# Kernel tuning notes

Measured on AMD Instinct MI355X. Metric: run time of the kernel, lower is better.

Reference implementation:

```python
import jax, jax.numpy as jnp
import numpy as np

ALPHA = 2
BETA = 4
# np.finfo(float64).eps threshold used in gaussian2D (max is always 1.0 at center)
EPS64 = 2.220446049250313e-16
CLIP = 1e-4


def _splat_level(boxes, labels, B, C, H, W):
    # boxes: [B,N,4] normalized cxcywh; labels: [B,N] int class ids
    # centers/radius in feature coordinates (scale_x*orig_w cancels to W)
    x = jnp.floor(boxes[..., 0] * W).astype(jnp.int32)           # [B,N]
    y = jnp.floor(boxes[..., 1] * H).astype(jnp.int32)
    bw = boxes[..., 2] * W
    bh = boxes[..., 3] * H
    r = jnp.maximum(1, jnp.floor((bw + bh) / 4.0).astype(jnp.int32))  # int() truncation, positive -> floor
    sigma = (2 * r + 1).astype(jnp.float32) / 6.0                # sigma = diameter/6

    dx = jnp.arange(W, dtype=jnp.int32)[None, None, :] - x[..., None]   # [B,N,W]
    dy = jnp.arange(H, dtype=jnp.int32)[None, None, :] - y[..., None]   # [B,N,H]
    d2 = (dx * dx)[:, :, None, :] + (dy * dy)[:, :, :, None]            # [B,N,H,W]
    g = jnp.exp(-d2.astype(jnp.float32) / (2.0 * sigma * sigma)[..., None, None])
    # window |d|<=r (border clipping is implicit since pixels lie in [0,W)x[0,H))
    inwin = (jnp.abs(dx) <= r[..., None])[:, :, None, :] & (jnp.abs(dy) <= r[..., None])[:, :, :, None]
    g = jnp.where(inwin & (g >= EPS64), g, 0.0)

    # scatter-max per (batch, label) channel
    N = boxes.shape[1]
    sid = (labels.astype(jnp.int32) + C * jnp.arange(B, dtype=jnp.int32)[:, None]).reshape(-1)  # [B*N]
    tm = jax.ops.segment_max(g.reshape(B * N, H * W), sid, num_segments=B * C)
    return jnp.maximum(tm, 0.0).reshape(B, C, H * W)  # empty segments (-inf) -> 0 init


def _forward(h0, h1, h2, boxes, labels):
    B, C = h0.shape[0], h0.shape[1]
    bx = jax.lax.stop_gradient(boxes)  # target construction is non-differentiable in the original
    maps = [h0, h1, h2]
    target = jnp.concatenate([_splat_level(bx, labels, B, C, m.shape[-2], m.shape[-1]) for m in maps], axis=2)
    heat = jnp.concatenate([m.reshape(B, C, -1) for m in maps], axis=2)

    pos = (target == 1.0).astype(heat.dtype)
    neg = (target < 1.0).astype(heat.dtype)
    neg_w = jnp.power(1.0 - target, BETA)
    p = jnp.clip(jax.nn.sigmoid(heat), CLIP, 1.0 - CLIP)
    pos_loss = jnp.log(p) * jnp.power(1.0 - p, ALPHA) * pos
    neg_loss = jnp.log(1.0 - p) * jnp.power(p, ALPHA) * neg_w * neg

    num_pos = pos.sum(axis=2, keepdims=True)
    pl = pos_loss.sum(axis=2, keepdims=True)
    nl = neg_loss.sum(axis=2, keepdims=True)
    safe = jnp.where(num_pos == 0, 1.0, num_pos)
    loss = jnp.where(num_pos == 0, -nl, -(pl + nl) / safe)
    loss = jnp.minimum(loss, 10.0)
    lm = jnp.log1p(loss.mean())
    return lm / (1.0 + lm)


def setup_inputs() -> dict:
    key = jax.random.key(0)
    k0, k1, k2, kb, kl = jax.random.split(key, 5)
    B, N, C = 8, 32, 80
    heat_map0 = jax.random.normal(k0, (B, C, 128, 128), dtype=jnp.float32)
    heat_map1 = jax.random.normal(k1, (B, C, 64, 64), dtype=jnp.float32)
    heat_map2 = jax.random.normal(k2, (B, C, 32, 32), dtype=jnp.float32)
    u = jax.random.uniform(kb, (B, N, 4), dtype=jnp.float32)
    boxes = jnp.concatenate([0.05 + 0.9 * u[..., :2], 0.02 + 0.4 * u[..., 2:]], axis=-1)
    labels = jax.random.randint(kl, (B, N), 0, C, dtype=jnp.int32)
    image_sizes = jnp.full((B, 2), 1024, dtype=jnp.int64)
    return {"heat_map0": heat_map0, "heat_map1": heat_map1, "heat_map2": heat_map2,
            "boxes": boxes, "labels": labels, "image_sizes": image_sizes}


def reference(heat_map0, heat_map1, heat_map2, boxes, labels, image_sizes):
    # image_sizes cancels out in the original math (scale_x * orig_w == feature W)
    return _forward(heat_map0, heat_map1, heat_map2, boxes, labels)
```

## Files before the change

### kernel.cpp

```cpp
#include <hip/hip_runtime.h>


#define BATCH 8
#define NBOX 32
#define NCH 80
#define NPLANE 640
#define NBLK 3840

__device__ __forceinline__ float sigmoid_clip(float h) {
    const float e = __expf(-h);
    float p = __builtin_amdgcn_rcpf(1.0f + e);
    return fminf(fmaxf(p, 1e-4f), 1.0f - 1e-4f);
}

__global__ __launch_bounds__(256) void splat_focal_kernel(
    const float* __restrict__ h0, const float* __restrict__ h1,
    const float* __restrict__ h2,
    const float* __restrict__ boxes, const int* __restrict__ labels,
    float* __restrict__ part)
{
    const int bid = blockIdx.x;
    const int tid = threadIdx.x;

    int plane, log2W, px_count, base_global, inpl_base;
    const float* heat;
    if (bid < 4 * NPLANE) {
        plane = bid >> 2;
        const int chunk = bid & 3;
        log2W = 7; heat = h0; px_count = 4096;
        inpl_base = chunk * 4096;
        base_global = plane * 16384 + inpl_base;
    } else if (bid < 5 * NPLANE) {
        plane = bid - 4 * NPLANE;
        log2W = 6; heat = h1; px_count = 4096;
        inpl_base = 0;
        base_global = plane * 4096;
    } else {
        plane = bid - 5 * NPLANE;
        log2W = 5; heat = h2; px_count = 1024;
        inpl_base = 0;
        base_global = plane * 1024;
    }
    const int W = 1 << log2W;
    const int b = plane / NCH;
    const int c = plane - b * NCH;

    __shared__ int s_k;
    __shared__ int s_x[NBOX], s_y[NBOX], s_r[NBOX];
    __shared__ float s_i2[NBOX];
    if (tid == 0) s_k = 0;
    __syncthreads();
    if (tid < NBOX) {
        if (labels[b * NBOX + tid] == c) {
            const float* bx = boxes + (b * NBOX + tid) * 4;
            const float fW = (float)W;
            int xi = (int)floorf(bx[0] * fW);
            int yi = (int)floorf(bx[1] * fW);
            int r = max(1, (int)floorf((bx[2] + bx[3]) * fW * 0.25f));
            float sigma = (float)(2 * r + 1) * (1.0f / 6.0f);
            int j = atomicAdd(&s_k, 1);
            s_x[j] = xi; s_y[j] = yi; s_r[j] = r;
            s_i2[j] = 1.0f / (2.0f * sigma * sigma);
        }
    }
    __syncthreads();
    const int k = s_k;

    float np_ = 0.0f, pl_ = 0.0f, nl_ = 0.0f;
    const int nf4 = px_count >> 2;
    const float4* hp = (const float4*)(heat + base_global);

    if (k == 0) {
        for (int i = tid; i < nf4; i += 256) {
            const float4 hq = hp[i];
            const float hv[4] = {hq.x, hq.y, hq.z, hq.w};
            #pragma unroll
            for (int j2 = 0; j2 < 4; ++j2) {
                const float p = sigmoid_clip(hv[j2]);
                nl_ += __logf(1.0f - p) * p * p;
            }
        }
    } else {
        for (int i = tid; i < nf4; i += 256) {
            const float4 hq = hp[i];
            const int off = inpl_base + (i << 2);
            const int py = off >> log2W;
            const int px0 = off & (W - 1);

            float t0 = 0.0f, t1 = 0.0f, t2 = 0.0f, t3 = 0.0f;
            for (int j = 0; j < k; ++j) {
                const int xj = s_x[j], yj = s_y[j], rj = s_r[j];
                const float i2 = s_i2[j];
                const int dy = py - yj;
                if (dy < -rj || dy > rj) continue;
                const float fdy2 = (float)(dy * dy);
                int dx = px0 - xj;
                if (dx >= -rj && dx <= rj)
                    t0 = fmaxf(t0, __expf(-((float)(dx * dx) + fdy2) * i2));
                dx += 1;
                if (dx >= -rj && dx <= rj)
                    t1 = fmaxf(t1, __expf(-((float)(dx * dx) + fdy2) * i2));
                dx += 1;
                if (dx >= -rj && dx <= rj)
                    t2 = fmaxf(t2, __expf(-((float)(dx * dx) + fdy2) * i2));
                dx += 1;
                if (dx >= -rj && dx <= rj)
                    t3 = fmaxf(t3, __expf(-((float)(dx * dx) + fdy2) * i2));
            }

            const float hv[4] = {hq.x, hq.y, hq.z, hq.w};
            const float tv[4] = {t0, t1, t2, t3};
            #pragma unroll
            for (int j2 = 0; j2 < 4; ++j2) {
                const float p = sigmoid_clip(hv[j2]);
                const float t = tv[j2];
                if (t == 1.0f) {
                    const float omp = 1.0f - p;
                    pl_ += __logf(p) * omp * omp;
                    np_ += 1.0f;
                } else {
                    const float omt = 1.0f - t;
                    const float nw = (omt * omt) * (omt * omt);
                    nl_ += __logf(1.0f - p) * p * p * nw;
                }
            }
        }
    }

    for (int o = 32; o > 0; o >>= 1) {
        np_ += __shfl_down(np_, o, 64);
        pl_ += __shfl_down(pl_, o, 64);
        nl_ += __shfl_down(nl_, o, 64);
    }
    __shared__ float s_np[4], s_pl[4], s_nl[4];
    const int wave = tid >> 6, lane = tid & 63;
    if (lane == 0) { s_np[wave] = np_; s_pl[wave] = pl_; s_nl[wave] = nl_; }
    __syncthreads();
    if (tid == 0) {
        part[bid]            = s_np[0] + s_np[1] + s_np[2] + s_np[3];
        part[NBLK + bid]     = s_pl[0] + s_pl[1] + s_pl[2] + s_pl[3];
        part[2 * NBLK + bid] = s_nl[0] + s_nl[1] + s_nl[2] + s_nl[3];
    }
}

__global__ __launch_bounds__(256) void finalize_kernel(
    const float* __restrict__ part, float* __restrict__ out)
{
    const int tid = threadIdx.x;
    const float* np = part;
    const float* pl = part + NBLK;
    const float* nl = part + 2 * NBLK;

    float s = 0.0f;
    for (int p = tid; p < NPLANE; p += 256) {
        const float4 n4 = ((const float4*)np)[p];
        const float4 p4 = ((const float4*)pl)[p];
        const float4 l4 = ((const float4*)nl)[p];
        const float a  = n4.x + n4.y + n4.z + n4.w + np[2560 + p] + np[3200 + p];
        const float ps = p4.x + p4.y + p4.z + p4.w + pl[2560 + p] + pl[3200 + p];
        const float ns = l4.x + l4.y + l4.z + l4.w + nl[2560 + p] + nl[3200 + p];
        const float loss = (a == 0.0f) ? (-ns) : (-(ps + ns) / a);
        s += fminf(loss, 10.0f);
    }
    for (int o = 32; o > 0; o >>= 1) s += __shfl_down(s, o, 64);
    __shared__ float sw[4];
    const int wave = tid >> 6, lane = tid & 63;
    if (lane == 0) sw[wave] = s;
    __syncthreads();
    if (tid == 0) {
        const float mean = (sw[0] + sw[1] + sw[2] + sw[3]) * (1.0f / (float)NPLANE);
        const float lm = log1pf(mean);
        out[0] = lm / (1.0f + lm);
    }
}

extern "C" void kernel_launch(void* const* d_in, const int* in_sizes, int n_in,
                              void* d_out, int out_size, void* d_ws, size_t ws_size,
                              hipStream_t stream) {
    const float* h0 = (const float*)d_in[0];
    const float* h1 = (const float*)d_in[1];
    const float* h2 = (const float*)d_in[2];
    const float* boxes = (const float*)d_in[3];
    const int* labels = (const int*)d_in[4];

    float* part = (float*)d_ws;

    splat_focal_kernel<<<NBLK, 256, 0, stream>>>(h0, h1, h2, boxes, labels, part);
    finalize_kernel<<<1, 256, 0, stream>>>(part, (float*)d_out);
}
```

Baseline: 101.5 us.

## Split dense negative-loss pass from sparse per-box window corrections

Every plane now runs a uniform streaming pass that computes only the unweighted negative term for all pixels. Separate per-box blocks visit just each box's window and add delta corrections for positive and weighted-negative pixels, using ownership by lowest box index to avoid double counting. The finalize kernel gathers the per-box corrections by label. This removes the per-pixel box loop and branch divergence from the dense pass, at the cost of more blocks, scattered window reads and recomputing box parameters inside the inner loop.

```diff
diff --git a/kernel.cpp b/kernel.cpp
--- a/kernel.cpp
+++ b/kernel.cpp
@@ -5,124 +5,117 @@
 #define NBOX 32
 #define NCH 80
 #define NPLANE 640
-#define NBLK 3840
 
-__device__ __forceinline__ float sigmoid_clip(float h) {
+__device__ __forceinline__ float sigclip(float h) {
     const float e = __expf(-h);
-    float p = __builtin_amdgcn_rcpf(1.0f + e);
+    const float p = __builtin_amdgcn_rcpf(1.0f + e);
     return fminf(fmaxf(p, 1e-4f), 1.0f - 1e-4f);
 }
+__device__ __forceinline__ float negterm(float h) {
+    const float p = sigclip(h);
+    return __logf(1.0f - p) * p * p;
+}
 
-__global__ __launch_bounds__(256) void splat_focal_kernel(
+__global__ __launch_bounds__(256) void hough_main_kernel(
     const float* __restrict__ h0, const float* __restrict__ h1,
     const float* __restrict__ h2,
     const float* __restrict__ boxes, const int* __restrict__ labels,
-    float* __restrict__ part)
+    float* __restrict__ ws)
 {
     const int bid = blockIdx.x;
     const int tid = threadIdx.x;
 
-    int plane, log2W, px_count, base_global, inpl_base;
-    const float* heat;
-    if (bid < 4 * NPLANE) {
-        plane = bid >> 2;
-        const int chunk = bid & 3;
-        log2W = 7; heat = h0; px_count = 4096;
-        inpl_base = chunk * 4096;
-        base_global = plane * 16384 + inpl_base;
-    } else if (bid < 5 * NPLANE) {
-        plane = bid - 4 * NPLANE;
-        log2W = 6; heat = h1; px_count = 4096;
-        inpl_base = 0;
-        base_global = plane * 4096;
-    } else {
-        plane = bid - 5 * NPLANE;
-        log2W = 5; heat = h2; px_count = 1024;
-        inpl_base = 0;
-        base_global = plane * 1024;
+    if (bid < 3840) {
+        const float* hp; int nf4; int slot;
+        if (bid < 2560) {
+            hp = h0 + ((size_t)bid << 12); nf4 = 1024; slot = bid;
+        } else if (bid < 3200) {
+            const int p = bid - 2560;
+            hp = h1 + ((size_t)p << 12); nf4 = 1024; slot = 2560 + p;
+        } else {
+            const int p = bid - 3200;
+            hp = h2 + ((size_t)p << 10); nf4 = 256; slot = 3200 + p;
+        }
+        const float4* f4 = (const float4*)hp;
+        float nl = 0.0f;
+        for (int i = tid; i < nf4; i += 256) {
+            const float4 q = f4[i];
+            nl += negterm(q.x) + negterm(q.y) + negterm(q.z) + negterm(q.w);
+        }
+        for (int o = 32; o > 0; o >>= 1) nl += __shfl_down(nl, o, 64);
+        __shared__ float sw[4];
+        const int w = tid >> 6, l = tid & 63;
+        if (l == 0) sw[w] = nl;
+        __syncthreads();
+        if (tid == 0) ws[slot] = sw[0] + sw[1] + sw[2] + sw[3];
+        return;
     }
-    const int W = 1 << log2W;
-    const int b = plane / NCH;
-    const int c = plane - b * NCH;
 
-    __shared__ int s_k;
-    __shared__ int s_x[NBOX], s_y[NBOX], s_r[NBOX];
-    __shared__ float s_i2[NBOX];
-    if (tid == 0) s_k = 0;
-    __syncthreads();
+    const int box = bid - 3840;
+    const int b = box >> 5, n = box & 31;
+
+    __shared__ float s_cx[NBOX], s_cy[NBOX], s_bw[NBOX], s_bh[NBOX];
+    __shared__ int s_lab[NBOX];
     if (tid < NBOX) {
-        if (labels[b * NBOX + tid] == c) {
-            const float* bx = boxes + (b * NBOX + tid) * 4;
-            const float fW = (float)W;
-            int xi = (int)floorf(bx[0] * fW);
-            int yi = (int)floorf(bx[1] * fW);
-            int r = max(1, (int)floorf((bx[2] + bx[3]) * fW * 0.25f));
-            float sigma = (float)(2 * r + 1) * (1.0f / 6.0f);
-            int j = atomicAdd(&s_k, 1);
-            s_x[j] = xi; s_y[j] = yi; s_r[j] = r;
-            s_i2[j] = 1.0f / (2.0f * sigma * sigma);
-        }
+        const float* bp = boxes + (size_t)(b * NBOX + tid) * 4;
+        s_cx[tid] = bp[0]; s_cy[tid] = bp[1];
+        s_bw[tid] = bp[2]; s_bh[tid] = bp[3];
+        s_lab[tid] = labels[b * NBOX + tid];
     }
     __syncthreads();
-    const int k = s_k;
 
-    float np_ = 0.0f, pl_ = 0.0f, nl_ = 0.0f;
-    const int nf4 = px_count >> 2;
-    const float4* hp = (const float4*)(heat + base_global);
+    const int c = s_lab[n];
+    float np_ = 0.0f, pl_ = 0.0f, nld = 0.0f;
+    const float* heats[3] = {h0, h1, h2};
 
-    if (k == 0) {
-        for (int i = tid; i < nf4; i += 256) {
-            const float4 hq = hp[i];
-            const float hv[4] = {hq.x, hq.y, hq.z, hq.w};
-            #pragma unroll
-            for (int j2 = 0; j2 < 4; ++j2) {
-                const float p = sigmoid_clip(hv[j2]);
-                nl_ += __logf(1.0f - p) * p * p;
+    for (int lv = 0; lv < 3; ++lv) {
+        const int lw = 7 - lv;
+        const int W = 1 << lw;
+        const float fW = (float)W;
+        const int xn = (int)floorf(s_cx[n] * fW);
+        const int yn = (int)floorf(s_cy[n] * fW);
+        int rn = (int)floorf((s_bw[n] * fW + s_bh[n] * fW) * 0.25f);
+        rn = max(1, rn);
+        const int wn = 2 * rn + 1;
+        const int tot = wn * wn;
+        const float* hb = heats[lv] + ((size_t)(b * NCH + c) << (2 * lw));
+
+        for (int idx = tid; idx < tot; idx += 256) {
+            const int dy = idx / wn;
+            const int dx = idx - dy * wn;
+            const int px = xn - rn + dx;
+            const int py = yn - rn + dy;
+            if (px < 0 || px >= W || py < 0 || py >= W) continue;
+
+            bool owned = true;
+            float t = 0.0f;
+            for (int m = 0; m < NBOX; ++m) {
+                if (s_lab[m] != c) continue;
+                const int xm = (int)floorf(s_cx[m] * fW);
+                const int ym = (int)floorf(s_cy[m] * fW);
+                int rm = (int)floorf((s_bw[m] * fW + s_bh[m] * fW) * 0.25f);
+                rm = max(1, rm);
+                const int ddx = px - xm, ddy = py - ym;
+                if (ddx < -rm || ddx > rm || ddy < -rm || ddy > rm) continue;
+                if (m < n) { owned = false; break; }
+                const float sig = (float)(2 * rm + 1) / 6.0f;
+                const float i2 = 1.0f / (2.0f * sig * sig);
+                t = fmaxf(t, __expf(-(float)(ddx * ddx + ddy * ddy) * i2));
             }
-        }
-    } else {
-        for (int i = tid; i < nf4; i += 256) {
-            const float4 hq = hp[i];
-            const int off = inpl_base + (i << 2);
-            const int py = off >> log2W;
-            const int px0 = off & (W - 1);
+            if (!owned) continue;
 
-            float t0 = 0.0f, t1 = 0.0f, t2 = 0.0f, t3 = 0.0f;
-            for (int j = 0; j < k; ++j) {
-                const int xj = s_x[j], yj = s_y[j], rj = s_r[j];
-                const float i2 = s_i2[j];
-                const int dy = py - yj;
-                if (dy < -rj || dy > rj) continue;
-                const float fdy2 = (float)(dy * dy);
-                int dx = px0 - xj;
-                if (dx >= -rj && dx <= rj)
-                    t0 = fmaxf(t0, __expf(-((float)(dx * dx) + fdy2) * i2));
-                dx += 1;
-                if (dx >= -rj && dx <= rj)
-                    t1 = fmaxf(t1, __expf(-((float)(dx * dx) + fdy2) * i2));
-                dx += 1;
-                if (dx >= -rj && dx <= rj)
-                    t2 = fmaxf(t2, __expf(-((float)(dx * dx) + fdy2) * i2));
-                dx += 1;
-                if (dx >= -rj && dx <= rj)
-                    t3 = fmaxf(t3, __expf(-((float)(dx * dx) + fdy2) * i2));
-            }
-
-            const float hv[4] = {hq.x, hq.y, hq.z, hq.w};
-            const float tv[4] = {t0, t1, t2, t3};
-            #pragma unroll
-            for (int j2 = 0; j2 < 4; ++j2) {
-                const float p = sigmoid_clip(hv[j2]);
-                const float t = tv[j2];
-                if (t == 1.0f) {
-                    const float omp = 1.0f - p;
-                    pl_ += __logf(p) * omp * omp;
-                    np_ += 1.0f;
-                } else {
-                    const float omt = 1.0f - t;
-                    const float nw = (omt * omt) * (omt * omt);
-                    nl_ += __logf(1.0f - p) * p * p * nw;
-                }
+            const float h = hb[py * W + px];
+            const float n0 = negterm(h);
+            if (t == 1.0f) {
+                const float p = sigclip(h);
+                const float omp = 1.0f - p;
+                pl_ += __logf(p) * omp * omp;
+                np_ += 1.0f;
+                nld -= n0;
+            } else {
+                const float omt = 1.0f - t;
+                const float nw4 = (omt * omt) * (omt * omt);
+                nld += n0 * (nw4 - 1.0f);
             }
         }
     }
@@ -130,42 +123,45 @@
     for (int o = 32; o > 0; o >>= 1) {
         np_ += __shfl_down(np_, o, 64);
         pl_ += __shfl_down(pl_, o, 64);
-        nl_ += __shfl_down(nl_, o, 64);
+        nld += __shfl_down(nld, o, 64);
     }
-    __shared__ float s_np[4], s_pl[4], s_nl[4];
-    const int wave = tid >> 6, lane = tid & 63;
-    if (lane == 0) { s_np[wave] = np_; s_pl[wave] = pl_; s_nl[wave] = nl_; }
+    __shared__ float r_np[4], r_pl[4], r_nl[4];
+    const int w = tid >> 6, l = tid & 63;
+    if (l == 0) { r_np[w] = np_; r_pl[w] = pl_; r_nl[w] = nld; }
     __syncthreads();
     if (tid == 0) {
-        part[bid]            = s_np[0] + s_np[1] + s_np[2] + s_np[3];
-        part[NBLK + bid]     = s_pl[0] + s_pl[1] + s_pl[2] + s_pl[3];
-        part[2 * NBLK + bid] = s_nl[0] + s_nl[1] + s_nl[2] + s_nl[3];
+        ws[3840 + box] = r_np[0] + r_np[1] + r_np[2] + r_np[3];
+        ws[4096 + box] = r_pl[0] + r_pl[1] + r_pl[2] + r_pl[3];
+        ws[4352 + box] = r_nl[0] + r_nl[1] + r_nl[2] + r_nl[3];
     }
 }
 
 __global__ __launch_bounds__(256) void finalize_kernel(
-    const float* __restrict__ part, float* __restrict__ out)
+    const float* __restrict__ ws, const int* __restrict__ labels,
+    float* __restrict__ out)
 {
     const int tid = threadIdx.x;
-    const float* np = part;
-    const float* pl = part + NBLK;
-    const float* nl = part + 2 * NBLK;
-
     float s = 0.0f;
     for (int p = tid; p < NPLANE; p += 256) {
-        const float4 n4 = ((const float4*)np)[p];
-        const float4 p4 = ((const float4*)pl)[p];
-        const float4 l4 = ((const float4*)nl)[p];
-        const float a  = n4.x + n4.y + n4.z + n4.w + np[2560 + p] + np[3200 + p];
-        const float ps = p4.x + p4.y + p4.z + p4.w + pl[2560 + p] + pl[3200 + p];
-        const float ns = l4.x + l4.y + l4.z + l4.w + nl[2560 + p] + nl[3200 + p];
-        const float loss = (a == 0.0f) ? (-ns) : (-(ps + ns) / a);
+        const int b = p / NCH, c = p - b * NCH;
+        const float4 n4 = ((const float4*)ws)[p];
+        float nl = n4.x + n4.y + n4.z + n4.w + ws[2560 + p] + ws[3200 + p];
+        float np_ = 0.0f, pl_ = 0.0f;
+        for (int m = 0; m < NBOX; ++m) {
+            if (labels[b * NBOX + m] == c) {
+                const int box = b * NBOX + m;
+                np_ += ws[3840 + box];
+                pl_ += ws[4096 + box];
+                nl  += ws[4352 + box];
+            }
+        }
+        const float loss = (np_ == 0.0f) ? (-nl) : (-(pl_ + nl) / np_);
         s += fminf(loss, 10.0f);
     }
     for (int o = 32; o > 0; o >>= 1) s += __shfl_down(s, o, 64);
     __shared__ float sw[4];
-    const int wave = tid >> 6, lane = tid & 63;
-    if (lane == 0) sw[wave] = s;
+    const int w = tid >> 6, l = tid & 63;
+    if (l == 0) sw[w] = s;
     __syncthreads();
     if (tid == 0) {
         const float mean = (sw[0] + sw[1] + sw[2] + sw[3]) * (1.0f / (float)NPLANE);
@@ -183,8 +179,8 @@
     const float* boxes = (const float*)d_in[3];
     const int* labels = (const int*)d_in[4];
 
-    float* part = (float*)d_ws;
+    float* ws = (float*)d_ws;
 
-    splat_focal_kernel<<<NBLK, 256, 0, stream>>>(h0, h1, h2, boxes, labels, part);
-    finalize_kernel<<<1, 256, 0, stream>>>(part, (float*)d_out);
+    hough_main_kernel<<<4096, 256, 0, stream>>>(h0, h1, h2, boxes, labels, ws);
+    finalize_kernel<<<1, 256, 0, stream>>>(ws, labels, (float*)d_out);
 }
```

New measurement: 171.5 us. 1.69x slower.
